# Performance work log

Hardware: AMD Instinct MI355X
Metric: run time of the kernel (lower is better)

Reference implementation:

```python
import jax, jax.numpy as jnp
import numpy as np

HID = 1024
HEADS = 16
HEAD_DIM = HID // HEADS


def setup_inputs() -> dict:
    key = jax.random.key(0)
    ks = jax.random.split(key, 12)
    B, S = 8, 1024
    s = 0.02
    return {
        "query": jax.random.normal(ks[0], (B, S, HID), jnp.float32),
        "key": jax.random.normal(ks[1], (B, S, HID), jnp.float32),
        "value": jax.random.normal(ks[2], (B, S, HID), jnp.float32),
        "Wq": jax.random.normal(ks[3], (HID, HID), jnp.float32) * s,
        "bq": jnp.zeros((HID,), jnp.float32),
        "Wk": jax.random.normal(ks[4], (HID, HID), jnp.float32) * s,
        "bk": jnp.zeros((HID,), jnp.float32),
        "Wv": jax.random.normal(ks[5], (HID, HID), jnp.float32) * s,
        "bv": jnp.zeros((HID,), jnp.float32),
        "Wo": jax.random.normal(ks[6], (HID, HID), jnp.float32) * s,
        "bo": jnp.zeros((HID,), jnp.float32),
        "mask": jnp.ones((B, 1, 1, S), jnp.int32),
    }


def _split_heads(x, B):
    # (B, S, HID) -> (B, H, S, D)
    return x.reshape(B, -1, HEADS, HEAD_DIM).transpose(0, 2, 1, 3)


def reference(query, key, value, Wq, bq, Wk, bk, Wv, bv, Wo, bo, mask):
    B = query.shape[0]
    scale = jnp.sqrt(jnp.float32(HEAD_DIM))
    Q = _split_heads(query @ Wq.T + bq, B)
    K = _split_heads(key @ Wk.T + bk, B)
    V = _split_heads(value @ Wv.T + bv, B)
    # energy: (B, H, Sq, Sk)
    energy = jnp.einsum("bhqd,bhkd->bhqk", Q, K) / scale
    energy = jnp.where(mask == 0, jnp.float32(-1e10), energy)
    attention = jax.nn.softmax(energy, axis=-1)
    # dropout is identity at inference
    x = jnp.einsum("bhqk,bhkd->bhqd", attention, V)
    x = x.transpose(0, 2, 1, 3).reshape(B, -1, HID)
    x = x @ Wo.T + bo
    return (x, attention)
```

## Files before the change

kernel.cpp:

```cpp
#include <hip/hip_runtime.h>
#include <cstdint>
#include <cstddef>


#define B_    8
#define S_    1024
#define HID_  1024
#define H_    16
#define D_    64
#define M_    (B_ * S_)

typedef __attribute__((ext_vector_type(8))) short bf16x8;
typedef __attribute__((ext_vector_type(4))) float f32x4;

#define ASYNC16(g, l)                                                     \
  __builtin_amdgcn_global_load_lds(                                       \
      (const __attribute__((address_space(1))) void*)(g),                 \
      (__attribute__((address_space(3))) void*)(l), 16, 0, 0)

__device__ __forceinline__ short f2bf(float f) {
  union { float f; uint32_t u; } v;
  v.f = f;
  uint32_t r = v.u + 0x7fffu + ((v.u >> 16) & 1u);
  return (short)(r >> 16);
}

__device__ __forceinline__ float bfbits2f(uint32_t bits) {
  union { uint32_t u; float f; } v;
  v.u = bits << 16;
  return v.f;
}

__global__ void cvt_f32_bf16(const float* __restrict__ in,
                             short* __restrict__ out, int n4) {
  int i = blockIdx.x * 256 + threadIdx.x;
  if (i >= n4) return;
  float4 v = ((const float4*)in)[i];
  ushort4 o;
  o.x = (unsigned short)f2bf(v.x);
  o.y = (unsigned short)f2bf(v.y);
  o.z = (unsigned short)f2bf(v.z);
  o.w = (unsigned short)f2bf(v.w);
  ((ushort4*)out)[i] = o;
}

__global__ __launch_bounds__(256) void qkv_proj(
    const short* __restrict__ xq, const short* __restrict__ xk,
    const short* __restrict__ xv, const short* __restrict__ wq,
    const short* __restrict__ wk, const short* __restrict__ wv,
    const float* __restrict__ bq, const float* __restrict__ bk,
    const float* __restrict__ bv, short* __restrict__ Qh,
    short* __restrict__ Kh, short* __restrict__ Vt) {
  const int z = blockIdx.z;
  const short* X = (z == 0) ? xq : (z == 1) ? xk : xv;
  const short* W = (z == 0) ? wq : (z == 1) ? wk : wv;
  const float* bias = (z == 0) ? bq : (z == 1) ? bk : bv;
  short* O = (z == 0) ? Qh : (z == 1) ? Kh : Vt;

  __shared__ __attribute__((aligned(16))) short As[128 * 32];
  __shared__ __attribute__((aligned(16))) short Bs[128 * 32];

  const int tid = threadIdx.x;
  const int lane = tid & 63, wave = tid >> 6;
  const int quad = lane >> 4, l16 = lane & 15;
  const int wr = (wave >> 1) * 64, wc = (wave & 1) * 64;
  const int m0 = blockIdx.y * 128, n0 = blockIdx.x * 128;

  f32x4 acc[4][4];
  for (int mi = 0; mi < 4; mi++)
    for (int ni = 0; ni < 4; ni++) acc[mi][ni] = (f32x4){0.f, 0.f, 0.f, 0.f};

  for (int k0 = 0; k0 < HID_; k0 += 32) {
#pragma unroll
    for (int i = 0; i < 2; i++) {
      int c = tid + i * 256;
      int row = c >> 2, co = (c & 3) * 8;
      ASYNC16(X + (size_t)(m0 + row) * HID_ + k0 + co, &As[c * 8]);
      ASYNC16(W + (size_t)(n0 + row) * HID_ + k0 + co, &Bs[c * 8]);
    }
    __syncthreads();

    bf16x8 af[4], bfr[4];
#pragma unroll
    for (int mi = 0; mi < 4; mi++)
      af[mi] = *(const bf16x8*)&As[(wr + mi * 16 + l16) * 32 + quad * 8];
#pragma unroll
    for (int ni = 0; ni < 4; ni++)
      bfr[ni] = *(const bf16x8*)&Bs[(wc + ni * 16 + l16) * 32 + quad * 8];
#pragma unroll
    for (int mi = 0; mi < 4; mi++)
#pragma unroll
      for (int ni = 0; ni < 4; ni++)
        acc[mi][ni] = __builtin_amdgcn_mfma_f32_16x16x32_bf16(
            af[mi], bfr[ni], acc[mi][ni], 0, 0, 0);
    __syncthreads();
  }

#pragma unroll
  for (int ni = 0; ni < 4; ni++) {
    int n = n0 + wc + ni * 16 + l16;
    float bn = bias[n];
    int h = n >> 6, d = n & 63;
#pragma unroll
    for (int mi = 0; mi < 4; mi++) {
      int mbase = m0 + wr + mi * 16 + quad * 4;
#pragma unroll
      for (int r = 0; r < 4; r++) {
        int m = mbase + r;
        int b = m >> 10, s = m & 1023;
        float v = acc[mi][ni][r] + bn;
        size_t o;
        if (z < 2)
          o = (((size_t)(b * H_ + h) * S_ + s) << 6) + d;
        else
          o = (((size_t)(b * H_ + h) * D_ + d) << 10) + s;
        O[o] = f2bf(v);
      }
    }
  }
}

__global__ __launch_bounds__(256) void out_proj(
    const short* __restrict__ X, const short* __restrict__ W,
    const float* __restrict__ bias, float* __restrict__ Out) {
  __shared__ __attribute__((aligned(16))) short As[128 * 32];
  __shared__ __attribute__((aligned(16))) short Bs[128 * 32];

  const int tid = threadIdx.x;
  const int lane = tid & 63, wave = tid >> 6;
  const int quad = lane >> 4, l16 = lane & 15;
  const int wr = (wave >> 1) * 64, wc = (wave & 1) * 64;
  const int m0 = blockIdx.y * 128, n0 = blockIdx.x * 128;

  f32x4 acc[4][4];
  for (int mi = 0; mi < 4; mi++)
    for (int ni = 0; ni < 4; ni++) acc[mi][ni] = (f32x4){0.f, 0.f, 0.f, 0.f};

  for (int k0 = 0; k0 < HID_; k0 += 32) {
#pragma unroll
    for (int i = 0; i < 2; i++) {
      int c = tid + i * 256;
      int row = c >> 2, co = (c & 3) * 8;
      ASYNC16(X + (size_t)(m0 + row) * HID_ + k0 + co, &As[c * 8]);
      ASYNC16(W + (size_t)(n0 + row) * HID_ + k0 + co, &Bs[c * 8]);
    }
    __syncthreads();
    bf16x8 af[4], bfr[4];
#pragma unroll
    for (int mi = 0; mi < 4; mi++)
      af[mi] = *(const bf16x8*)&As[(wr + mi * 16 + l16) * 32 + quad * 8];
#pragma unroll
    for (int ni = 0; ni < 4; ni++)
      bfr[ni] = *(const bf16x8*)&Bs[(wc + ni * 16 + l16) * 32 + quad * 8];
#pragma unroll
    for (int mi = 0; mi < 4; mi++)
#pragma unroll
      for (int ni = 0; ni < 4; ni++)
        acc[mi][ni] = __builtin_amdgcn_mfma_f32_16x16x32_bf16(
            af[mi], bfr[ni], acc[mi][ni], 0, 0, 0);
    __syncthreads();
  }

#pragma unroll
  for (int ni = 0; ni < 4; ni++) {
    int n = n0 + wc + ni * 16 + l16;
    float bn = bias[n];
#pragma unroll
    for (int mi = 0; mi < 4; mi++) {
      int mbase = m0 + wr + mi * 16 + quad * 4;
#pragma unroll
      for (int r = 0; r < 4; r++)
        Out[(size_t)(mbase + r) * HID_ + n] = acc[mi][ni][r] + bn;
    }
  }
}

__global__ __launch_bounds__(256, 2) void attn_kernel(
    const short* __restrict__ Qh, const short* __restrict__ Kh,
    const short* __restrict__ Vt, const int* __restrict__ mask,
    float* __restrict__ attn_out, short* __restrict__ ctx) {
  const int qt = blockIdx.x;
  const int bh = blockIdx.y;
  const int b = bh >> 4, h = bh & 15;

  const short* Qp = Qh + ((size_t)bh << 16);
  const short* Kp = Kh + ((size_t)bh << 16);
  const short* Vp = Vt + ((size_t)bh << 16);
  float* Ap = attn_out + ((size_t)bh << 20);
  const int* mp = mask + b * S_;

  __shared__ __attribute__((aligned(16))) short Ks[64 * 64];
  __shared__ __attribute__((aligned(16))) short Vs[64 * 64];
  __shared__ __attribute__((aligned(16))) short Ps[4][16 * 64];
  __shared__ int Ms[S_];

  const int tid = threadIdx.x;
  const int lane = tid & 63, wave = tid >> 6;
  const int quad = lane >> 4, l16 = lane & 15;
  const float scale = 0.125f;

  for (int i = tid; i < S_; i += 256) Ms[i] = mp[i];

  bf16x8 aq[2];
  {
    const short* qrow = Qp + (size_t)(qt * 64 + wave * 16 + l16) * D_;
    aq[0] = *(const bf16x8*)(qrow + quad * 8);
    aq[1] = *(const bf16x8*)(qrow + 32 + quad * 8);
  }
  __syncthreads();

  float l_lane[4] = {0.f, 0.f, 0.f, 0.f};
  f32x4 acc[4];
#pragma unroll
  for (int n = 0; n < 4; n++) acc[n] = (f32x4){0.f, 0.f, 0.f, 0.f};

  uint32_t pk[16][4][2];

#pragma unroll
  for (int kt = 0; kt < 16; kt++) {
#pragma unroll
    for (int i = 0; i < 2; i++) {
      int c = tid + i * 256;
      int row = c >> 3;
      int sl = (c & 7) ^ (row & 7);
      ASYNC16(Kp + (size_t)(kt * 64 + row) * D_ + sl * 8, &Ks[c * 8]);
      ASYNC16(Vp + (size_t)row * S_ + kt * 64 + sl * 8, &Vs[c * 8]);
    }
    __syncthreads();

#pragma unroll
    for (int nt = 0; nt < 4; nt++) {
      f32x4 sv = (f32x4){0.f, 0.f, 0.f, 0.f};
      const int krow = nt * 16 + l16;
      const int kswz = (krow & 7) << 3;
#pragma unroll
      for (int s = 0; s < 2; s++) {
        bf16x8 kb =
            *(const bf16x8*)&Ks[krow * 64 + ((s * 32 + quad * 8) ^ kswz)];
        sv = __builtin_amdgcn_mfma_f32_16x16x32_bf16(aq[s], kb, sv, 0, 0, 0);
      }
      int mv = Ms[kt * 64 + nt * 16 + l16];
      unsigned short pb[4];
#pragma unroll
      for (int r = 0; r < 4; r++) {
        float x = mv ? sv[r] * scale : -1e10f;
        float p = __expf(x);
        l_lane[r] += p;
        pb[r] = (unsigned short)f2bf(p);
        int prow = quad * 4 + r;
        Ps[wave][prow * 64 + ((nt * 16 + l16) ^ ((prow & 7) << 3))] =
            (short)pb[r];
      }
      pk[kt][nt][0] = (uint32_t)pb[0] | ((uint32_t)pb[1] << 16);
      pk[kt][nt][1] = (uint32_t)pb[2] | ((uint32_t)pb[3] << 16);
    }

#pragma unroll
    for (int s = 0; s < 2; s++) {
      bf16x8 pa = *(const bf16x8*)&Ps[wave][l16 * 64 +
                                           ((s * 32 + quad * 8) ^
                                            ((l16 & 7) << 3))];
#pragma unroll
      for (int nt2 = 0; nt2 < 4; nt2++) {
        const int vrow = nt2 * 16 + l16;
        bf16x8 vb =
            *(const bf16x8*)&Vs[vrow * 64 +
                                ((s * 32 + quad * 8) ^ ((vrow & 7) << 3))];
        acc[nt2] =
            __builtin_amdgcn_mfma_f32_16x16x32_bf16(pa, vb, acc[nt2], 0, 0, 0);
      }
    }
    __syncthreads();
  }

  float inv_l[4];
#pragma unroll
  for (int r = 0; r < 4; r++) {
    float s = l_lane[r];
#pragma unroll
    for (int off = 1; off < 16; off <<= 1) s += __shfl_xor(s, off, 64);
    inv_l[r] = 1.0f / s;
  }

#pragma unroll
  for (int nt2 = 0; nt2 < 4; nt2++) {
#pragma unroll
    for (int r = 0; r < 4; r++) {
      int q = qt * 64 + wave * 16 + quad * 4 + r;
      ctx[((size_t)(b * S_ + q)) * HID_ + h * D_ + nt2 * 16 + l16] =
          f2bf(acc[nt2][r] * inv_l[r]);
    }
  }

  const int qrow0 = qt * 64 + wave * 16 + quad * 4;
#pragma unroll
  for (int kt = 0; kt < 16; kt++) {
#pragma unroll
    for (int nt = 0; nt < 4; nt++) {
      uint32_t lo = pk[kt][nt][0], hi = pk[kt][nt][1];
      float p0 = bfbits2f(lo & 0xffffu);
      float p1 = bfbits2f(lo >> 16);
      float p2 = bfbits2f(hi & 0xffffu);
      float p3 = bfbits2f(hi >> 16);
      float* base = Ap + (size_t)qrow0 * S_ + kt * 64 + nt * 16 + l16;
      base[0 * S_] = p0 * inv_l[0];
      base[1 * S_] = p1 * inv_l[1];
      base[2 * S_] = p2 * inv_l[2];
      base[3 * S_] = p3 * inv_l[3];
    }
  }
}

extern "C" void kernel_launch(void* const* d_in, const int* in_sizes, int n_in,
                              void* d_out, int out_size, void* d_ws,
                              size_t ws_size, hipStream_t stream) {
  const float* query = (const float*)d_in[0];
  const float* key   = (const float*)d_in[1];
  const float* value = (const float*)d_in[2];
  const float* Wq = (const float*)d_in[3];
  const float* bq = (const float*)d_in[4];
  const float* Wk = (const float*)d_in[5];
  const float* bk = (const float*)d_in[6];
  const float* Wv = (const float*)d_in[7];
  const float* bv = (const float*)d_in[8];
  const float* Wo = (const float*)d_in[9];
  const float* bo = (const float*)d_in[10];
  const int* mask = (const int*)d_in[11];

  float* out_x = (float*)d_out;
  float* out_attn = out_x + (size_t)M_ * HID_;

  char* w = (char*)d_ws;
  const size_t XB = (size_t)M_ * HID_ * 2;
  const size_t WB = (size_t)HID_ * HID_ * 2;
  short* xq = (short*)w;              w += XB;
  short* xk = (short*)w;              w += XB;
  short* xv = (short*)w;              w += XB;
  short* wqb = (short*)w;             w += WB;
  short* wkb = (short*)w;             w += WB;
  short* wvb = (short*)w;             w += WB;
  short* wob = (short*)w;             w += WB;
  short* Qh = (short*)w;              w += XB;
  short* Kh = (short*)w;              w += XB;
  short* Vt = (short*)w;              w += XB;
  short* ctx = (short*)w;             w += XB;

  cvt_f32_bf16<<<(M_ * HID_ / 4 + 255) / 256, 256, 0, stream>>>(query, xq, M_ * HID_ / 4);
  cvt_f32_bf16<<<(M_ * HID_ / 4 + 255) / 256, 256, 0, stream>>>(key, xk, M_ * HID_ / 4);
  cvt_f32_bf16<<<(M_ * HID_ / 4 + 255) / 256, 256, 0, stream>>>(value, xv, M_ * HID_ / 4);
  cvt_f32_bf16<<<(HID_ * HID_ / 4 + 255) / 256, 256, 0, stream>>>(Wq, wqb, HID_ * HID_ / 4);
  cvt_f32_bf16<<<(HID_ * HID_ / 4 + 255) / 256, 256, 0, stream>>>(Wk, wkb, HID_ * HID_ / 4);
  cvt_f32_bf16<<<(HID_ * HID_ / 4 + 255) / 256, 256, 0, stream>>>(Wv, wvb, HID_ * HID_ / 4);
  cvt_f32_bf16<<<(HID_ * HID_ / 4 + 255) / 256, 256, 0, stream>>>(Wo, wob, HID_ * HID_ / 4);

  qkv_proj<<<dim3(HID_ / 128, M_ / 128, 3), 256, 0, stream>>>(
      xq, xk, xv, wqb, wkb, wvb, bq, bk, bv, Qh, Kh, Vt);

  attn_kernel<<<dim3(S_ / 64, B_ * H_), 256, 0, stream>>>(
      Qh, Kh, Vt, mask, out_attn, ctx);

  out_proj<<<dim3(HID_ / 128, M_ / 128), 256, 0, stream>>>(ctx, wob, bo, out_x);
}
```

Before: 891.8 us.

## Fuse conversions, use 128-key tiles, stage attention rows in LDS

Merges the seven f32-to-bf16 conversion launches into one grid-stride kernel. Widens the attention key tile from 64 to 128, which halves the number of loop iterations and barriers. Stages each normalized attention-probability row through LDS so the probabilities are written to global memory as contiguous float4 rows instead of scattered 4-byte stores. The cost is more LDS per block, which may reduce occupancy, plus LDS round-trip traffic and waits in the epilogue.

```diff
diff --git a/kernel.cpp b/kernel.cpp
--- a/kernel.cpp
+++ b/kernel.cpp
@@ -31,17 +31,34 @@
   return v.f;
 }
 
-__global__ void cvt_f32_bf16(const float* __restrict__ in,
-                             short* __restrict__ out, int n4) {
-  int i = blockIdx.x * 256 + threadIdx.x;
-  if (i >= n4) return;
-  float4 v = ((const float4*)in)[i];
-  ushort4 o;
-  o.x = (unsigned short)f2bf(v.x);
-  o.y = (unsigned short)f2bf(v.y);
-  o.z = (unsigned short)f2bf(v.z);
-  o.w = (unsigned short)f2bf(v.w);
-  ((ushort4*)out)[i] = o;
+__global__ __launch_bounds__(256) void cvt_all(
+    const float* __restrict__ q, const float* __restrict__ k,
+    const float* __restrict__ v, const float* __restrict__ Wq,
+    const float* __restrict__ Wk, const float* __restrict__ Wv,
+    const float* __restrict__ Wo, short* __restrict__ xq,
+    short* __restrict__ xk, short* __restrict__ xv, short* __restrict__ wq,
+    short* __restrict__ wk, short* __restrict__ wv, short* __restrict__ wo) {
+  const float* in;
+  short* out;
+  int n4;
+  switch (blockIdx.y) {
+    case 0: in = q;  out = xq; n4 = M_ * HID_ / 4; break;
+    case 1: in = k;  out = xk; n4 = M_ * HID_ / 4; break;
+    case 2: in = v;  out = xv; n4 = M_ * HID_ / 4; break;
+    case 3: in = Wq; out = wq; n4 = HID_ * HID_ / 4; break;
+    case 4: in = Wk; out = wk; n4 = HID_ * HID_ / 4; break;
+    case 5: in = Wv; out = wv; n4 = HID_ * HID_ / 4; break;
+    default: in = Wo; out = wo; n4 = HID_ * HID_ / 4; break;
+  }
+  for (int i = blockIdx.x * 256 + threadIdx.x; i < n4; i += gridDim.x * 256) {
+    float4 vv = ((const float4*)in)[i];
+    ushort4 o;
+    o.x = (unsigned short)f2bf(vv.x);
+    o.y = (unsigned short)f2bf(vv.y);
+    o.z = (unsigned short)f2bf(vv.z);
+    o.w = (unsigned short)f2bf(vv.w);
+    ((ushort4*)out)[i] = o;
+  }
 }
 
 __global__ __launch_bounds__(256) void qkv_proj(
@@ -189,10 +206,12 @@
   float* Ap = attn_out + ((size_t)bh << 20);
   const int* mp = mask + b * S_;
 
-  __shared__ __attribute__((aligned(16))) short Ks[64 * 64];
-  __shared__ __attribute__((aligned(16))) short Vs[64 * 64];
-  __shared__ __attribute__((aligned(16))) short Ps[4][16 * 64];
+  __shared__ __attribute__((aligned(16))) short KVS[128 * 64 + 64 * 128];
+  __shared__ __attribute__((aligned(16))) short Ps[4][16 * 128];
   __shared__ int Ms[S_];
+
+  short* const Ks = KVS;
+  short* const Vs = KVS + 128 * 64;
 
   const int tid = threadIdx.x;
   const int lane = tid & 63, wave = tid >> 6;
@@ -214,22 +233,22 @@
 #pragma unroll
   for (int n = 0; n < 4; n++) acc[n] = (f32x4){0.f, 0.f, 0.f, 0.f};
 
-  uint32_t pk[16][4][2];
-
-#pragma unroll
-  for (int kt = 0; kt < 16; kt++) {
-#pragma unroll
-    for (int i = 0; i < 2; i++) {
+  uint32_t pk[8][8][2];
+
+#pragma unroll
+  for (int kt = 0; kt < 8; kt++) {
+#pragma unroll
+    for (int i = 0; i < 4; i++) {
       int c = tid + i * 256;
-      int row = c >> 3;
-      int sl = (c & 7) ^ (row & 7);
-      ASYNC16(Kp + (size_t)(kt * 64 + row) * D_ + sl * 8, &Ks[c * 8]);
-      ASYNC16(Vp + (size_t)row * S_ + kt * 64 + sl * 8, &Vs[c * 8]);
-    }
-    __syncthreads();
-
-#pragma unroll
-    for (int nt = 0; nt < 4; nt++) {
+      int krow = c >> 3, kc = (c & 7) ^ (krow & 7);
+      ASYNC16(Kp + (size_t)(kt * 128 + krow) * D_ + kc * 8, &Ks[c * 8]);
+      int vrow = c >> 4, vc = (c & 15) ^ (vrow & 7);
+      ASYNC16(Vp + (size_t)vrow * S_ + kt * 128 + vc * 8, &Vs[c * 8]);
+    }
+    __syncthreads();
+
+#pragma unroll
+    for (int nt = 0; nt < 8; nt++) {
       f32x4 sv = (f32x4){0.f, 0.f, 0.f, 0.f};
       const int krow = nt * 16 + l16;
       const int kswz = (krow & 7) << 3;
@@ -239,7 +258,7 @@
             *(const bf16x8*)&Ks[krow * 64 + ((s * 32 + quad * 8) ^ kswz)];
         sv = __builtin_amdgcn_mfma_f32_16x16x32_bf16(aq[s], kb, sv, 0, 0, 0);
       }
-      int mv = Ms[kt * 64 + nt * 16 + l16];
+      int mv = Ms[kt * 128 + nt * 16 + l16];
       unsigned short pb[4];
 #pragma unroll
       for (int r = 0; r < 4; r++) {
@@ -248,7 +267,7 @@
         l_lane[r] += p;
         pb[r] = (unsigned short)f2bf(p);
         int prow = quad * 4 + r;
-        Ps[wave][prow * 64 + ((nt * 16 + l16) ^ ((prow & 7) << 3))] =
+        Ps[wave][prow * 128 + ((nt * 16 + l16) ^ ((prow & 7) << 3))] =
             (short)pb[r];
       }
       pk[kt][nt][0] = (uint32_t)pb[0] | ((uint32_t)pb[1] << 16);
@@ -256,16 +275,16 @@
     }
 
 #pragma unroll
-    for (int s = 0; s < 2; s++) {
-      bf16x8 pa = *(const bf16x8*)&Ps[wave][l16 * 64 +
-                                           ((s * 32 + quad * 8) ^
+    for (int ks = 0; ks < 4; ks++) {
+      bf16x8 pa = *(const bf16x8*)&Ps[wave][l16 * 128 +
+                                           ((ks * 32 + quad * 8) ^
                                             ((l16 & 7) << 3))];
 #pragma unroll
       for (int nt2 = 0; nt2 < 4; nt2++) {
         const int vrow = nt2 * 16 + l16;
         bf16x8 vb =
-            *(const bf16x8*)&Vs[vrow * 64 +
-                                ((s * 32 + quad * 8) ^ ((vrow & 7) << 3))];
+            *(const bf16x8*)&Vs[vrow * 128 +
+                                ((ks * 32 + quad * 8) ^ ((vrow & 7) << 3))];
         acc[nt2] =
             __builtin_amdgcn_mfma_f32_16x16x32_bf16(pa, vb, acc[nt2], 0, 0, 0);
       }
@@ -292,21 +311,29 @@
     }
   }
 
-  const int qrow0 = qt * 64 + wave * 16 + quad * 4;
-#pragma unroll
-  for (int kt = 0; kt < 16; kt++) {
-#pragma unroll
-    for (int nt = 0; nt < 4; nt++) {
-      uint32_t lo = pk[kt][nt][0], hi = pk[kt][nt][1];
-      float p0 = bfbits2f(lo & 0xffffu);
-      float p1 = bfbits2f(lo >> 16);
-      float p2 = bfbits2f(hi & 0xffffu);
-      float p3 = bfbits2f(hi >> 16);
-      float* base = Ap + (size_t)qrow0 * S_ + kt * 64 + nt * 16 + l16;
-      base[0 * S_] = p0 * inv_l[0];
-      base[1 * S_] = p1 * inv_l[1];
-      base[2 * S_] = p2 * inv_l[2];
-      base[3 * S_] = p3 * inv_l[3];
+  float* const Es = ((float*)KVS) + wave * 1024;
+#pragma unroll
+  for (int r16 = 0; r16 < 16; r16++) {
+    const int qsel = r16 >> 2, r = r16 & 3;
+    asm volatile("s_waitcnt lgkmcnt(0)" ::: "memory");
+    if (quad == qsel) {
+      const float il = inv_l[r];
+#pragma unroll
+      for (int kt = 0; kt < 8; kt++)
+#pragma unroll
+        for (int nt = 0; nt < 8; nt++) {
+          uint32_t w32 = pk[kt][nt][r >> 1];
+          float pv = bfbits2f((r & 1) ? (w32 >> 16) : (w32 & 0xffffu));
+          Es[kt * 128 + nt * 16 + l16] = pv * il;
+        }
+    }
+    asm volatile("s_waitcnt lgkmcnt(0)" ::: "memory");
+    const int qrow = qt * 64 + wave * 16 + r16;
+    float* dst = Ap + (size_t)qrow * S_;
+#pragma unroll
+    for (int j = 0; j < 4; j++) {
+      float4 f = *(const float4*)&Es[j * 256 + lane * 4];
+      *(float4*)&dst[j * 256 + lane * 4] = f;
     }
   }
 }
@@ -345,13 +372,8 @@
   short* Vt = (short*)w;              w += XB;
   short* ctx = (short*)w;             w += XB;
 
-  cvt_f32_bf16<<<(M_ * HID_ / 4 + 255) / 256, 256, 0, stream>>>(query, xq, M_ * HID_ / 4);
-  cvt_f32_bf16<<<(M_ * HID_ / 4 + 255) / 256, 256, 0, stream>>>(key, xk, M_ * HID_ / 4);
-  cvt_f32_bf16<<<(M_ * HID_ / 4 + 255) / 256, 256, 0, stream>>>(value, xv, M_ * HID_ / 4);
-  cvt_f32_bf16<<<(HID_ * HID_ / 4 + 255) / 256, 256, 0, stream>>>(Wq, wqb, HID_ * HID_ / 4);
-  cvt_f32_bf16<<<(HID_ * HID_ / 4 + 255) / 256, 256, 0, stream>>>(Wk, wkb, HID_ * HID_ / 4);
-  cvt_f32_bf16<<<(HID_ * HID_ / 4 + 255) / 256, 256, 0, stream>>>(Wv, wvb, HID_ * HID_ / 4);
-  cvt_f32_bf16<<<(HID_ * HID_ / 4 + 255) / 256, 256, 0, stream>>>(Wo, wob, HID_ * HID_ / 4);
+  cvt_all<<<dim3(2048, 7), 256, 0, stream>>>(
+      query, key, value, Wq, Wk, Wv, Wo, xq, xk, xv, wqb, wkb, wvb, wob);
 
   qkv_proj<<<dim3(HID_ / 128, M_ / 128, 3), 256, 0, stream>>>(
       xq, xk, xv, wqb, wkb, wvb, bq, bk, bv, Qh, Kh, Vt);
```

After: 911.0 us. 1.02x slower.
